# Optimization experiments

Measured on AMD Instinct MI355X. Metric: run time of the kernel, lower is better.

The kernel has to match this reference:

```python
import jax, jax.numpy as jnp
import numpy as np

# Dimensions (AlphaFold-scale IPA / GeometricFrameAttention)
B, N = 1, 768
C_S, C_Z, C_H, H, PQ, PV = 384, 128, 16, 12, 4, 8
INF = 1e9
EPS = 1e-8
SOFTPLUS_INV_1 = 0.541324854612918  # gfa_point_weights_init_


def quat_to_rot(q):
    """Unit-normalize quaternions [..., 4] -> rotation matrices [..., 3, 3]."""
    q = q / jnp.linalg.norm(q, axis=-1, keepdims=True)
    w, x, y, z = q[..., 0], q[..., 1], q[..., 2], q[..., 3]
    R = jnp.stack([
        1 - 2 * (y * y + z * z), 2 * (x * y - w * z), 2 * (x * z + w * y),
        2 * (x * y + w * z), 1 - 2 * (x * x + z * z), 2 * (y * z - w * x),
        2 * (x * z - w * y), 2 * (y * z + w * x), 1 - 2 * (x * x + y * y),
    ], axis=-1)
    return R.reshape(q.shape[:-1] + (3, 3))


def setup_inputs() -> dict:
    key = jax.random.key(0)
    ks = jax.random.split(key, 12)

    def lin(k, out_d, in_d):
        return jax.random.normal(k, (out_d, in_d), jnp.float32) * (1.0 / np.sqrt(in_d))

    out_in = H * C_H + H * PV * 4 + H * C_Z  # o + o_pt(x,y,z) + o_pt_norm + o_pair
    inp = {
        "s": jax.random.normal(ks[0], (B, N, C_S), jnp.float32),
        "z": jax.random.normal(ks[1], (B, N, N, C_Z), jnp.float32),
        "rot": quat_to_rot(jax.random.normal(ks[2], (B, N, 4), jnp.float32)),
        "trans": jax.random.normal(ks[3], (B, N, 3), jnp.float32),
        "mask": jnp.ones((B, N), jnp.float32),
        "Wq": lin(ks[4], H * C_H, C_S),
        "bq": jnp.zeros((H * C_H,), jnp.float32),
        "Wkv": lin(ks[5], H * 2 * C_H, C_S),
        "bkv": jnp.zeros((H * 2 * C_H,), jnp.float32),
        "Wqp": lin(ks[6], H * PQ * 3, C_S),
        "bqp": jnp.zeros((H * PQ * 3,), jnp.float32),
        "Wkvp": lin(ks[7], H * (PQ + PV) * 3, C_S),
        "bkvp": jnp.zeros((H * (PQ + PV) * 3,), jnp.float32),
        "Wb": lin(ks[8], H, C_Z),
        "bb": jnp.zeros((H,), jnp.float32),
        "head_w": jnp.full((H,), SOFTPLUS_INV_1, jnp.float32),
        "Wout": lin(ks[9], C_S, out_in),
        "bout": jnp.zeros((C_S,), jnp.float32),
    }
    return inp


def _forward(s, z, rot, trans, mask, Wq, bq, Wkv, bkv, Wqp, bqp, Wkvp, bkvp,
             Wb, bb, head_w, Wout, bout):
    Bn, Nn, _ = s.shape
    # scalar q/k/v
    q = (s @ Wq.T + bq).reshape(Bn, Nn, H, C_H)
    kv = (s @ Wkv.T + bkv).reshape(Bn, Nn, H, 2 * C_H)
    k, v = kv[..., :C_H], kv[..., C_H:]
    # point q/k/v: local frame -> global frame (x_glob = R x_loc + t)
    q_pts = (s @ Wqp.T + bqp).reshape(Bn, Nn, H * PQ, 3)
    q_pts = (jnp.einsum('bnxy,bnpy->bnpx', rot, q_pts) + trans[:, :, None]).reshape(Bn, Nn, H, PQ, 3)
    kv_pts = (s @ Wkvp.T + bkvp).reshape(Bn, Nn, H * (PQ + PV), 3)
    kv_pts = (jnp.einsum('bnxy,bnpy->bnpx', rot, kv_pts) + trans[:, :, None]).reshape(Bn, Nn, H, PQ + PV, 3)
    k_pts, v_pts = kv_pts[..., :PQ, :], kv_pts[..., PQ:, :]
    # pair bias [B,N,N,H] -> [B,H,N,N]
    bias = z @ Wb.T + bb
    a = jnp.einsum('bihc,bjhc->bhij', q, k) * np.float32(np.sqrt(1.0 / (3 * C_H)))
    a = a + np.float32(np.sqrt(1.0 / 3.0)) * jnp.transpose(bias, (0, 3, 1, 2))
    # point distance term: sum_p |q_p - k_p|^2 = |q|^2 + |k|^2 - 2 q.k (no [B,N,N,H,P,3] tensor)
    q2 = jnp.sum(q_pts ** 2, axis=(-1, -2))  # [B,N,H]
    k2 = jnp.sum(k_pts ** 2, axis=(-1, -2))
    qk = jnp.einsum('bihpc,bjhpc->bhij', q_pts, k_pts)
    d2 = q2.transpose(0, 2, 1)[..., :, None] + k2.transpose(0, 2, 1)[..., None, :] - 2.0 * qk
    hw = jax.nn.softplus(head_w) * np.float32(np.sqrt(2.0 / (27.0 * PQ)))  # sqrt(1/(3*(PQ*9/2)))
    a = a - 0.5 * hw[None, :, None, None] * d2
    # mask bias
    sq_mask = mask[..., :, None] * mask[..., None, :]
    a = a + (INF * (sq_mask - 1.0))[:, None]
    a = jax.nn.softmax(a, axis=-1)  # [B,H,N,N]
    # outputs
    o = jnp.einsum('bhij,bjhc->bihc', a, v).reshape(Bn, Nn, H * C_H)
    o_pt = jnp.einsum('bhij,bjhpc->bihpc', a, v_pts)  # global frame
    o_pt = jnp.einsum('bnyx,bnhpy->bnhpx', rot, o_pt - trans[:, :, None, None])  # back to local
    o_pt_norm = jnp.sqrt(jnp.sum(o_pt ** 2, axis=-1) + EPS).reshape(Bn, Nn, H * PV)
    o_pt_flat = jnp.moveaxis(o_pt, -1, -3).reshape(Bn, Nn, 3 * H * PV)  # coord-major like unbind+cat
    o_pair = jnp.einsum('bhij,bijc->bihc', a, z).reshape(Bn, Nn, H * C_Z)
    cat = jnp.concatenate([o, o_pt_flat, o_pt_norm, o_pair], axis=-1)
    return cat @ Wout.T + bout


def reference(s, z, rot, trans, mask, Wq, bq, Wkv, bkv, Wqp, bqp, Wkvp, bkvp,
              Wb, bb, head_w, Wout, bout):
    return _forward(s, z, rot, trans, mask, Wq, bq, Wkv, bkv, Wqp, bqp,
                    Wkvp, bkvp, Wb, bb, head_w, Wout, bout)
```

## Files before the change

### kernel.cpp

```cpp
#include <hip/hip_runtime.h>
#include <math.h>

#define NN 768
#define CS 384
#define CZ 128
#define CH 16
#define HH 12
#define PQ 4
#define PV 8
#define OUTIN 2112

#define SC_QK 0.14433756729740643f
#define SC_B  0.57735026918962576f
#define SC_HW 0.13608276348795434f
#define MSLACK 12.0f

__device__ __forceinline__ float dpp_add(float x, const int ctrl) {
    int yi;
    switch (ctrl) {
        case 0: yi = __builtin_amdgcn_update_dpp(0, __float_as_int(x), 0xB1,  0xf, 0xf, true); break;
        case 1: yi = __builtin_amdgcn_update_dpp(0, __float_as_int(x), 0x4E,  0xf, 0xf, true); break;
        case 2: yi = __builtin_amdgcn_update_dpp(0, __float_as_int(x), 0x141, 0xf, 0xf, true); break;
        default:yi = __builtin_amdgcn_update_dpp(0, __float_as_int(x), 0x140, 0xf, 0xf, true); break;
    }
    return x + __int_as_float(yi);
}
__device__ __forceinline__ float dpp_max(float x, const int ctrl) {
    int yi;
    switch (ctrl) {
        case 0: yi = __builtin_amdgcn_update_dpp(0, __float_as_int(x), 0xB1,  0xf, 0xf, true); break;
        case 1: yi = __builtin_amdgcn_update_dpp(0, __float_as_int(x), 0x4E,  0xf, 0xf, true); break;
        case 2: yi = __builtin_amdgcn_update_dpp(0, __float_as_int(x), 0x141, 0xf, 0xf, true); break;
        default:yi = __builtin_amdgcn_update_dpp(0, __float_as_int(x), 0x140, 0xf, 0xf, true); break;
    }
    return fmaxf(x, __int_as_float(yi));
}

__global__ __launch_bounds__(256) void kproj(
    const float* __restrict__ s,
    const float* __restrict__ Wq,  const float* __restrict__ bq,
    const float* __restrict__ Wkv, const float* __restrict__ bkv,
    const float* __restrict__ Wqp, const float* __restrict__ bqp,
    const float* __restrict__ Wkvp,const float* __restrict__ bkvp,
    float* __restrict__ q, float* __restrict__ kT, float* __restrict__ vall,
    float* __restrict__ qpr, float* __restrict__ kvpr)
{
    __shared__ float s_lds[8*384];
    int n0 = blockIdx.x * 8;
    int t = threadIdx.x;
    for (int idx = t; idx < 8*384; idx += 256)
        s_lds[idx] = s[(n0 + idx/384)*384 + (idx%384)];
    __syncthreads();

    int o = blockIdx.y * 128 + (t & 127);
    int ng = t >> 7;
    const float* wrow; float bias;
    if (o < 192)      { wrow = Wq   + o*384;       bias = bq[o]; }
    else if (o < 576) { wrow = Wkv  + (o-192)*384; bias = bkv[o-192]; }
    else if (o < 720) { wrow = Wqp  + (o-576)*384; bias = bqp[o-576]; }
    else              { wrow = Wkvp + (o-720)*384; bias = bkvp[o-720]; }

    float acc[4] = {bias, bias, bias, bias};
    const float4* wr4 = reinterpret_cast<const float4*>(wrow);
    for (int c4 = 0; c4 < 96; ++c4) {
        float4 w = wr4[c4];
        #pragma unroll
        for (int nn = 0; nn < 4; ++nn) {
            const float* sr = &s_lds[(ng*4+nn)*384 + c4*4];
            acc[nn] = fmaf(w.x, sr[0], acc[nn]);
            acc[nn] = fmaf(w.y, sr[1], acc[nn]);
            acc[nn] = fmaf(w.z, sr[2], acc[nn]);
            acc[nn] = fmaf(w.w, sr[3], acc[nn]);
        }
    }
    #pragma unroll
    for (int nn = 0; nn < 4; ++nn) {
        int n = n0 + ng*4 + nn;
        float v = acc[nn];
        if (o < 192)      q[n*192 + o] = v;
        else if (o < 576) {
            int oo = o - 192, h = oo >> 5, cc = oo & 31;
            if (cc < 16) kT[(h*NN + n)*16 + cc] = v;
            else         vall[(size_t)n*480 + h*40 + (cc-16)] = v;
        }
        else if (o < 720) qpr[n*144 + (o-576)] = v;
        else              kvpr[n*432 + (o-720)] = v;
    }
}

__global__ __launch_bounds__(192) void krot(
    const float* __restrict__ rot, const float* __restrict__ trans,
    const float* __restrict__ qpr, const float* __restrict__ kvpr,
    float* __restrict__ qp, float* __restrict__ kpT, float* __restrict__ vall)
{
    int n = blockIdx.x;
    __shared__ float R[9], T[3];
    int t = threadIdx.x;
    if (t < 9) R[t] = rot[n*9 + t];
    if (t < 3) T[t] = trans[n*3 + t];
    __syncthreads();

    const float* src = (t < 48) ? (qpr + n*144 + t*3) : (kvpr + n*432 + (t-48)*3);
    float x = src[0], y = src[1], z = src[2];
    float wx = R[0]*x + R[1]*y + R[2]*z + T[0];
    float wy = R[3]*x + R[4]*y + R[5]*z + T[1];
    float wz = R[6]*x + R[7]*y + R[8]*z + T[2];
    if (t < 48) {
        float* d = qp + n*144 + t*3;
        d[0]=wx; d[1]=wy; d[2]=wz;
    } else {
        int pi = t - 48, h = pi/12, pp = pi%12;
        if (pp < 4) {
            float* d = kpT + (h*NN+n)*12 + pp*3;
            d[0]=wx; d[1]=wy; d[2]=wz;
        } else {
            float* d = vall + (size_t)n*480 + h*40 + 16 + (pp-4)*3;
            d[0]=wx; d[1]=wy; d[2]=wz;
        }
    }
}

__global__ __launch_bounds__(256) void kqk(
    const float* __restrict__ kT, const float* __restrict__ kpT,
    const float* __restrict__ q, const float* __restrict__ qp,
    const float* __restrict__ mask, const float* __restrict__ head_w,
    const float* __restrict__ bb, float* __restrict__ lqd,
    float* __restrict__ mpart)
{
    const int j0 = blockIdx.x * 64;
    const int i0 = blockIdx.y * 32;
    __shared__ float ktl[64][17], kpl[64][13];
    __shared__ float ql[32][17],  qpl[32][13];
    __shared__ float mi_l[32], mj_l[64];
    __shared__ float mpl[32][12];
    const int t = threadIdx.x;
    if (t < 32) mi_l[t] = mask[i0 + t];
    if (t < 64) mj_l[t] = mask[j0 + t];

    const int jl = t & 63, wv = t >> 6;

    for (int h = 0; h < 12; ++h) {
        __syncthreads();
        for (int idx = t; idx < 1024; idx += 256)
            ktl[idx >> 4][idx & 15] = kT[(size_t)(h*NN + j0 + (idx >> 4))*16 + (idx & 15)];
        for (int idx = t; idx < 768; idx += 256) {
            int r = idx / 12, e = idx - r*12;
            kpl[r][e] = kpT[(size_t)(h*NN + j0 + r)*12 + e];
        }
        for (int idx = t; idx < 512; idx += 256)
            ql[idx >> 4][idx & 15] = q[(i0 + (idx >> 4))*192 + h*16 + (idx & 15)];
        for (int idx = t; idx < 384; idx += 256) {
            int r = idx / 12, e = idx - r*12;
            qpl[r][e] = qp[(i0 + r)*144 + h*12 + e];
        }
        __syncthreads();

        const float hwh = log1pf(expf(head_w[h])) * SC_HW;
        const float bbh = bb[h] * SC_B;
        const float mj = mj_l[jl];
        #pragma unroll
        for (int k = 0; k < 8; ++k) {
            const int il = wv*8 + k;
            float qk = 0.f;
            #pragma unroll
            for (int c = 0; c < 16; ++c) qk = fmaf(ktl[jl][c], ql[il][c], qk);
            float d2 = 0.f;
            #pragma unroll
            for (int e = 0; e < 12; ++e) { float d = qpl[il][e] - kpl[jl][e]; d2 = fmaf(d, d, d2); }
            float mt = 1e9f * (mi_l[il]*mj - 1.0f);
            float lg = fmaf(qk, SC_QK, fmaf(-0.5f*hwh, d2, bbh)) + mt;
            lqd[((size_t)(i0+il)*NN + j0 + jl)*12 + h] = lg;
            float m = lg;
            m = dpp_max(m, 0);
            m = dpp_max(m, 1);
            m = dpp_max(m, 2);
            m = dpp_max(m, 3);
            m = fmaxf(m, __shfl_xor(m, 16, 64));
            m = fmaxf(m, __shfl_xor(m, 32, 64));
            if (jl == 0) mpl[il][h] = m;
        }
    }
    __syncthreads();
    if (t < 384) {
        int il = t / 12, h = t - il*12;
        mpart[((size_t)h*NN + i0 + il)*12 + blockIdx.x] = mpl[il][h];
    }
}

__global__ __launch_bounds__(256) void kfuse(
    const float* __restrict__ z, const float* __restrict__ Wb,
    const float* __restrict__ lqd, const float* __restrict__ mpart,
    const float* __restrict__ vall,
    float* __restrict__ opart, float* __restrict__ vpart, float* __restrict__ ssum)
{
    __shared__ float  M_lds[12];
    __shared__ __align__(16) float p_lds[12][68];
    __shared__ float2 ofold[4][12][64];
    __shared__ float  sredL[16][6];

    const int i = blockIdx.x, jseg = blockIdx.y;
    const int t = threadIdx.x, w = t >> 6, l = t & 63;
    const int gid = t >> 4, cl = t & 15;
    const int hhalf = gid & 1, h0 = hhalf * 6, jofs = gid >> 1;

    if (t < 12) {
        const float4* mp = (const float4*)(mpart + ((size_t)t*NN + i)*12);
        float4 a = mp[0], b = mp[1], c = mp[2];
        float m = fmaxf(fmaxf(fmaxf(a.x,a.y), fmaxf(a.z,a.w)),
                 fmaxf(fmaxf(fmaxf(b.x,b.y), fmaxf(b.z,b.w)),
                       fmaxf(fmaxf(c.x,c.y), fmaxf(c.z,c.w))));
        M_lds[t] = m + MSLACK;
    }

    float4 wva[6], wvb[6];
    #pragma unroll
    for (int h = 0; h < 6; ++h) {
        const float4* wp = (const float4*)(Wb + (h0+h)*CZ + cl*8);
        wva[h] = wp[0]; wvb[h] = wp[1];
    }

    float2 oa[12];
    #pragma unroll
    for (int h = 0; h < 12; ++h) { oa[h].x = 0.f; oa[h].y = 0.f; }
    float2 vacc; vacc.x = 0.f; vacc.y = 0.f;
    const int vch = 2*t;
    const int vh  = (t < 240) ? (vch / 40) : 0;
    float s_acc = 0.f;

    __syncthreads();
    const float Mh = M_lds[h0 + (cl < 6 ? cl : 5)];
    const int jbase = jseg * 384;

    for (int tile = 0; tile < 6; ++tile) {
        const int jt = jbase + tile*64;

        {
            const float4* zq0 = (const float4*)(z + ((size_t)i*NN + jt + jofs)*CZ) + cl*2;
            float4 za = zq0[0], zb = zq0[1];
            for (int it = 0; it < 8; ++it) {
                float4 zaN = za, zbN = zb;
                if (it + 1 < 8) {
                    const float4* zq = (const float4*)(z + ((size_t)i*NN + jt + (it+1)*8 + jofs)*CZ) + cl*2;
                    zaN = zq[0]; zbN = zq[1];
                }
                const int j = jt + it*8 + jofs;
                float b0, b1, b2, b3, b4, b5;
                #define BDOT(BV, H)                                \
                    BV = za.x*wva[H].x;                            \
                    BV = fmaf(za.y, wva[H].y, BV);                 \
                    BV = fmaf(za.z, wva[H].z, BV);                 \
                    BV = fmaf(za.w, wva[H].w, BV);                 \
                    BV = fmaf(zb.x, wvb[H].x, BV);                 \
                    BV = fmaf(zb.y, wvb[H].y, BV);                 \
                    BV = fmaf(zb.z, wvb[H].z, BV);                 \
                    BV = fmaf(zb.w, wvb[H].w, BV);
                BDOT(b0, 0) BDOT(b1, 1) BDOT(b2, 2) BDOT(b3, 3) BDOT(b4, 4) BDOT(b5, 5)
                #undef BDOT
                #define BRED(BV)                                   \
                    BV = dpp_add(BV, 0);                           \
                    BV = dpp_add(BV, 1);                           \
                    BV = dpp_add(BV, 2);                           \
                    BV = dpp_add(BV, 3);
                BRED(b0) BRED(b1) BRED(b2) BRED(b3) BRED(b4) BRED(b5)
                #undef BRED
                float bsel = b0;
                bsel = (cl == 1) ? b1 : bsel;
                bsel = (cl == 2) ? b2 : bsel;
                bsel = (cl == 3) ? b3 : bsel;
                bsel = (cl == 4) ? b4 : bsel;
                bsel = (cl == 5) ? b5 : bsel;
                if (cl < 6) {
                    float g = fmaf(bsel, SC_B, lqd[((size_t)i*NN + j)*12 + h0 + cl]);
                    float p = __expf(g - Mh);
                    p_lds[h0 + cl][j - jt] = p;
                    s_acc += p;
                }
                za = zaN; zb = zbN;
            }
        }
        __syncthreads();

        {
            const float2* zr2 = (const float2*)(z + (size_t)i*NN*CZ) + l;
            #pragma unroll 4
            for (int jj = 0; jj < 16; ++jj) {
                const int jb = jj*4 + w;
                float2 zv = zr2[(size_t)(jt + jb)*64];
                #pragma unroll
                for (int h = 0; h < 12; ++h) {
                    float pv = p_lds[h][jb];
                    oa[h].x = fmaf(pv, zv.x, oa[h].x);
                    oa[h].y = fmaf(pv, zv.y, oa[h].y);
                }
            }
        }

        if (t < 240) {
            const float2* vr = (const float2*)(vall + (size_t)jt*480 + vch);
            #pragma unroll 4
            for (int q4 = 0; q4 < 16; ++q4) {
                float4 pv = *(const float4*)&p_lds[vh][q4*4];
                float2 v0 = vr[(size_t)(q4*4+0)*240];
                float2 v1 = vr[(size_t)(q4*4+1)*240];
                float2 v2 = vr[(size_t)(q4*4+2)*240];
                float2 v3 = vr[(size_t)(q4*4+3)*240];
                vacc.x = fmaf(pv.x, v0.x, vacc.x); vacc.y = fmaf(pv.x, v0.y, vacc.y);
                vacc.x = fmaf(pv.y, v1.x, vacc.x); vacc.y = fmaf(pv.y, v1.y, vacc.y);
                vacc.x = fmaf(pv.z, v2.x, vacc.x); vacc.y = fmaf(pv.z, v2.y, vacc.y);
                vacc.x = fmaf(pv.w, v3.x, vacc.x); vacc.y = fmaf(pv.w, v3.y, vacc.y);
            }
        }
        __syncthreads();
    }

    #pragma unroll
    for (int h = 0; h < 12; ++h) ofold[w][h][l] = oa[h];
    if (cl < 6) sredL[gid][cl] = s_acc;
    if (t < 240)
        *((float2*)(vpart + ((size_t)(jseg*NN + i))*480) + t) = vacc;
    __syncthreads();

    float2* opw = (float2*)(opart + ((size_t)(jseg*NN + i))*1536);
    #pragma unroll
    for (int k = 0; k < 3; ++k) {
        int slot = k*256 + t;
        int h = slot >> 6, c2 = slot & 63;
        float2 v0 = ofold[0][h][c2], v1 = ofold[1][h][c2];
        float2 v2 = ofold[2][h][c2], v3 = ofold[3][h][c2];
        float2 o;
        o.x = v0.x + v1.x + v2.x + v3.x;
        o.y = v0.y + v1.y + v2.y + v3.y;
        opw[slot] = o;
    }
    if (t < 12) {
        float sv = 0.f;
        #pragma unroll
        for (int k = 0; k < 8; ++k) sv += sredL[k*2 + (t/6)][t % 6];
        ssum[(size_t)(jseg*12 + t)*NN + i] = sv;
    }
}

__global__ __launch_bounds__(256) void kepi(
    const float* __restrict__ opart, const float* __restrict__ vpart,
    const float* __restrict__ ssum, const float* __restrict__ rot,
    const float* __restrict__ trans, float* __restrict__ cat)
{
    __shared__ float sinv[12];
    __shared__ float optl[12][24];
    __shared__ float R[9], T[3];
    const int i = blockIdx.x, t = threadIdx.x;
    if (t < 9) R[t] = rot[i*9 + t];
    if (t < 3) T[t] = trans[i*3 + t];
    if (t >= 16 && t < 28) {
        int h = t - 16;
        sinv[h] = 1.0f / (ssum[(size_t)h*NN + i] + ssum[(size_t)(12+h)*NN + i]);
    }
    __syncthreads();

    float* crow = cat + (size_t)i*OUTIN;
    const float2* op0 = (const float2*)(opart + (size_t)i*1536);
    const float2* op1 = (const float2*)(opart + (size_t)(NN + i)*1536);
    #pragma unroll
    for (int k = 0; k < 3; ++k) {
        int slot = k*256 + t;
        int h = slot >> 6, c2 = slot & 63;
        float2 a = op0[slot], b = op1[slot];
        float sc = sinv[h];
        float2 o; o.x = (a.x + b.x)*sc; o.y = (a.y + b.y)*sc;
        *(float2*)(crow + 576 + h*128 + c2*2) = o;
    }
    if (t < 240) {
        const int ch = 2*t, h = ch/40, e = ch%40;
        float2 v0 = *(const float2*)(vpart + (size_t)i*480 + ch);
        float2 v1 = *(const float2*)(vpart + (size_t)(NN + i)*480 + ch);
        float sc = sinv[h];
        float vx = (v0.x + v1.x)*sc, vy = (v0.y + v1.y)*sc;
        if (e < 16) { crow[h*16 + e] = vx; crow[h*16 + e + 1] = vy; }
        else        { optl[h][e-16] = vx; optl[h][e-15] = vy; }
    }
    __syncthreads();
    if (t < 96) {
        int h = t >> 3, pp = t & 7;
        float wx = optl[h][pp*3+0] - T[0];
        float wy = optl[h][pp*3+1] - T[1];
        float wz = optl[h][pp*3+2] - T[2];
        crow[192 + 0*96 + h*8 + pp] = R[0]*wx + R[3]*wy + R[6]*wz;
        crow[192 + 1*96 + h*8 + pp] = R[1]*wx + R[4]*wy + R[7]*wz;
        crow[192 + 2*96 + h*8 + pp] = R[2]*wx + R[5]*wy + R[8]*wz;
        crow[480 + h*8 + pp] = sqrtf(fmaf(wx,wx,fmaf(wy,wy,wz*wz)) + 1e-8f);
    }
}

__global__ __launch_bounds__(256) void koutp(
    const float* __restrict__ cat, const float* __restrict__ Wout,
    float* __restrict__ ptmp)
{
    __shared__ float ct[32][36];
    __shared__ float wt[64][36];
    const int n0 = blockIdx.x * 32, o0 = blockIdx.y * 64;
    const int k0 = blockIdx.z * 352;
    const int t = threadIdx.x;
    const int tn = (t >> 4) * 2;
    const int to = t & 15;

    float a00=0,a01=0,a02=0,a03=0, a10=0,a11=0,a12=0,a13=0;

    for (int c = 0; c < 11; ++c) {
        __syncthreads();
        #pragma unroll
        for (int u = 0; u < 4; ++u) {
            int idx = u*256 + t, r = idx >> 5, cc = idx & 31;
            ct[r][cc] = cat[(size_t)(n0 + r)*OUTIN + k0 + c*32 + cc];
        }
        #pragma unroll
        for (int u = 0; u < 8; ++u) {
            int idx = u*256 + t, r = idx >> 5, cc = idx & 31;
            wt[r][cc] = Wout[(size_t)(o0 + r)*OUTIN + k0 + c*32 + cc];
        }
        __syncthreads();
        #pragma unroll
        for (int kk = 0; kk < 32; kk += 4) {
            float4 c0 = *(const float4*)&ct[tn][kk];
            float4 c1 = *(const float4*)&ct[tn+1][kk];
            float4 w0 = *(const float4*)&wt[to][kk];
            float4 w1 = *(const float4*)&wt[to+16][kk];
            float4 w2 = *(const float4*)&wt[to+32][kk];
            float4 w3 = *(const float4*)&wt[to+48][kk];
            a00 = fmaf(c0.x,w0.x,a00); a00 = fmaf(c0.y,w0.y,a00); a00 = fmaf(c0.z,w0.z,a00); a00 = fmaf(c0.w,w0.w,a00);
            a01 = fmaf(c0.x,w1.x,a01); a01 = fmaf(c0.y,w1.y,a01); a01 = fmaf(c0.z,w1.z,a01); a01 = fmaf(c0.w,w1.w,a01);
            a02 = fmaf(c0.x,w2.x,a02); a02 = fmaf(c0.y,w2.y,a02); a02 = fmaf(c0.z,w2.z,a02); a02 = fmaf(c0.w,w2.w,a02);
            a03 = fmaf(c0.x,w3.x,a03); a03 = fmaf(c0.y,w3.y,a03); a03 = fmaf(c0.z,w3.z,a03); a03 = fmaf(c0.w,w3.w,a03);
            a10 = fmaf(c1.x,w0.x,a10); a10 = fmaf(c1.y,w0.y,a10); a10 = fmaf(c1.z,w0.z,a10); a10 = fmaf(c1.w,w0.w,a10);
            a11 = fmaf(c1.x,w1.x,a11); a11 = fmaf(c1.y,w1.y,a11); a11 = fmaf(c1.z,w1.z,a11); a11 = fmaf(c1.w,w1.w,a11);
            a12 = fmaf(c1.x,w2.x,a12); a12 = fmaf(c1.y,w2.y,a12); a12 = fmaf(c1.z,w2.z,a12); a12 = fmaf(c1.w,w2.w,a12);
            a13 = fmaf(c1.x,w3.x,a13); a13 = fmaf(c1.y,w3.y,a13); a13 = fmaf(c1.z,w3.z,a13); a13 = fmaf(c1.w,w3.w,a13);
        }
    }
    float* pb = ptmp + (size_t)blockIdx.z * (NN*384);
    pb[(size_t)(n0+tn+0)*384 + o0+to+ 0] = a00;
    pb[(size_t)(n0+tn+0)*384 + o0+to+16] = a01;
    pb[(size_t)(n0+tn+0)*384 + o0+to+32] = a02;
    pb[(size_t)(n0+tn+0)*384 + o0+to+48] = a03;
    pb[(size_t)(n0+tn+1)*384 + o0+to+ 0] = a10;
    pb[(size_t)(n0+tn+1)*384 + o0+to+16] = a11;
    pb[(size_t)(n0+tn+1)*384 + o0+to+32] = a12;
    pb[(size_t)(n0+tn+1)*384 + o0+to+48] = a13;
}

__global__ __launch_bounds__(256) void kred(
    const float* __restrict__ ptmp, const float* __restrict__ bout,
    float* __restrict__ out)
{
    int idx = blockIdx.x * 256 + threadIdx.x;
    int o = idx % 384;
    float v = bout[o];
    #pragma unroll
    for (int s = 0; s < 6; ++s) v += ptmp[(size_t)s*(NN*384) + idx];
    out[idx] = v;
}

extern "C" void kernel_launch(void* const* d_in, const int* in_sizes, int n_in,
                              void* d_out, int out_size, void* d_ws, size_t ws_size,
                              hipStream_t stream) {
    const float* s      = (const float*)d_in[0];
    const float* z      = (const float*)d_in[1];
    const float* rot    = (const float*)d_in[2];
    const float* trans  = (const float*)d_in[3];
    const float* mask   = (const float*)d_in[4];
    const float* Wq     = (const float*)d_in[5];
    const float* bq     = (const float*)d_in[6];
    const float* Wkv    = (const float*)d_in[7];
    const float* bkv    = (const float*)d_in[8];
    const float* Wqp    = (const float*)d_in[9];
    const float* bqp    = (const float*)d_in[10];
    const float* Wkvp   = (const float*)d_in[11];
    const float* bkvp   = (const float*)d_in[12];
    const float* Wb     = (const float*)d_in[13];
    const float* bb     = (const float*)d_in[14];
    const float* head_w = (const float*)d_in[15];
    const float* Wout   = (const float*)d_in[16];
    const float* bout   = (const float*)d_in[17];
    float* out = (float*)d_out;
    float* ws  = (float*)d_ws;

    float* q     = ws;
    float* kT    = ws + 147456;
    float* kpT   = ws + 294912;
    float* vall  = ws + 405504;
    float* qp    = ws + 774144;
    float* qpr   = ws + 884736;
    float* kvpr  = ws + 995328;
    float* mpart = ws + 1327104;
    float* ssum  = ws + 1437696;
    float* cat   = ws + 1456128;
    float* lqd   = ws + 3078144;
    float* opart = ws + 10156032;
    float* vpart = ws + 12515328;
    float* ptmp  = ws + 13252608;

    kproj<<<dim3(96, 9), 256, 0, stream>>>(s, Wq, bq, Wkv, bkv, Wqp, bqp, Wkvp, bkvp,
                                           q, kT, vall, qpr, kvpr);
    krot<<<dim3(768), 192, 0, stream>>>(rot, trans, qpr, kvpr, qp, kpT, vall);
    kqk<<<dim3(12, 24), 256, 0, stream>>>(kT, kpT, q, qp, mask, head_w, bb, lqd, mpart);
    kfuse<<<dim3(768, 2), 256, 0, stream>>>(z, Wb, lqd, mpart, vall, opart, vpart, ssum);
    kepi<<<dim3(768), 256, 0, stream>>>(opart, vpart, ssum, rot, trans, cat);
    koutp<<<dim3(24, 6, 6), 256, 0, stream>>>(cat, Wout, ptmp);
    kred<<<dim3(1152), 256, 0, stream>>>(ptmp, bout, out);
}
```

Before: 402.0 us.

## Split kfuse over four j-segments and read transposed probabilities as float4

The fused pair-bias/softmax/aggregation kernel now splits the key dimension into four segments of 192 instead of two of 384, which doubles the grid to 3072 blocks. The epilogue now sums four partial outputs and four partial row sums. Probabilities are also written to a transposed LDS buffer, so the z-aggregation loop reads them with three float4 loads instead of twelve scalar loads. The workspace layout is reordered to fit the larger partial buffers, with ptmp aliased onto lqd. The trade-offs are more partial-sum traffic in kepi, extra LDS stores, and more LDS per block.

After: 411.2 us. 2.3% more time.

```diff
diff --git a/kernel.cpp b/kernel.cpp
--- a/kernel.cpp
+++ b/kernel.cpp
@@ -195,6 +195,7 @@
 {
     __shared__ float  M_lds[12];
     __shared__ __align__(16) float p_lds[12][68];
+    __shared__ __align__(16) float p_T[64][16];
     __shared__ float2 ofold[4][12][64];
     __shared__ float  sredL[16][6];
 
@@ -229,9 +230,9 @@
 
     __syncthreads();
     const float Mh = M_lds[h0 + (cl < 6 ? cl : 5)];
-    const int jbase = jseg * 384;
-
-    for (int tile = 0; tile < 6; ++tile) {
+    const int jbase = jseg * 192;
+
+    for (int tile = 0; tile < 3; ++tile) {
         const int jt = jbase + tile*64;
 
         {
@@ -273,6 +274,7 @@
                     float g = fmaf(bsel, SC_B, lqd[((size_t)i*NN + j)*12 + h0 + cl]);
                     float p = __expf(g - Mh);
                     p_lds[h0 + cl][j - jt] = p;
+                    p_T[j - jt][h0 + cl] = p;
                     s_acc += p;
                 }
                 za = zaN; zb = zbN;
@@ -286,12 +288,21 @@
             for (int jj = 0; jj < 16; ++jj) {
                 const int jb = jj*4 + w;
                 float2 zv = zr2[(size_t)(jt + jb)*64];
-                #pragma unroll
-                for (int h = 0; h < 12; ++h) {
-                    float pv = p_lds[h][jb];
-                    oa[h].x = fmaf(pv, zv.x, oa[h].x);
-                    oa[h].y = fmaf(pv, zv.y, oa[h].y);
-                }
+                float4 pA = *(const float4*)&p_T[jb][0];
+                float4 pB = *(const float4*)&p_T[jb][4];
+                float4 pC = *(const float4*)&p_T[jb][8];
+                oa[0].x  = fmaf(pA.x, zv.x, oa[0].x);  oa[0].y  = fmaf(pA.x, zv.y, oa[0].y);
+                oa[1].x  = fmaf(pA.y, zv.x, oa[1].x);  oa[1].y  = fmaf(pA.y, zv.y, oa[1].y);
+                oa[2].x  = fmaf(pA.z, zv.x, oa[2].x);  oa[2].y  = fmaf(pA.z, zv.y, oa[2].y);
+                oa[3].x  = fmaf(pA.w, zv.x, oa[3].x);  oa[3].y  = fmaf(pA.w, zv.y, oa[3].y);
+                oa[4].x  = fmaf(pB.x, zv.x, oa[4].x);  oa[4].y  = fmaf(pB.x, zv.y, oa[4].y);
+                oa[5].x  = fmaf(pB.y, zv.x, oa[5].x);  oa[5].y  = fmaf(pB.y, zv.y, oa[5].y);
+                oa[6].x  = fmaf(pB.z, zv.x, oa[6].x);  oa[6].y  = fmaf(pB.z, zv.y, oa[6].y);
+                oa[7].x  = fmaf(pB.w, zv.x, oa[7].x);  oa[7].y  = fmaf(pB.w, zv.y, oa[7].y);
+                oa[8].x  = fmaf(pC.x, zv.x, oa[8].x);  oa[8].y  = fmaf(pC.x, zv.y, oa[8].y);
+                oa[9].x  = fmaf(pC.y, zv.x, oa[9].x);  oa[9].y  = fmaf(pC.y, zv.y, oa[9].y);
+                oa[10].x = fmaf(pC.z, zv.x, oa[10].x); oa[10].y = fmaf(pC.z, zv.y, oa[10].y);
+                oa[11].x = fmaf(pC.w, zv.x, oa[11].x); oa[11].y = fmaf(pC.w, zv.y, oa[11].y);
             }
         }
 
@@ -353,28 +364,36 @@
     if (t < 3) T[t] = trans[i*3 + t];
     if (t >= 16 && t < 28) {
         int h = t - 16;
-        sinv[h] = 1.0f / (ssum[(size_t)h*NN + i] + ssum[(size_t)(12+h)*NN + i]);
+        sinv[h] = 1.0f / (ssum[(size_t)h*NN + i] + ssum[(size_t)(12+h)*NN + i]
+                        + ssum[(size_t)(24+h)*NN + i] + ssum[(size_t)(36+h)*NN + i]);
     }
     __syncthreads();
 
     float* crow = cat + (size_t)i*OUTIN;
     const float2* op0 = (const float2*)(opart + (size_t)i*1536);
     const float2* op1 = (const float2*)(opart + (size_t)(NN + i)*1536);
+    const float2* op2 = (const float2*)(opart + (size_t)(2*NN + i)*1536);
+    const float2* op3 = (const float2*)(opart + (size_t)(3*NN + i)*1536);
     #pragma unroll
     for (int k = 0; k < 3; ++k) {
         int slot = k*256 + t;
         int h = slot >> 6, c2 = slot & 63;
-        float2 a = op0[slot], b = op1[slot];
+        float2 a = op0[slot], b = op1[slot], c = op2[slot], d = op3[slot];
         float sc = sinv[h];
-        float2 o; o.x = (a.x + b.x)*sc; o.y = (a.y + b.y)*sc;
+        float2 o;
+        o.x = (a.x + b.x + c.x + d.x)*sc;
+        o.y = (a.y + b.y + c.y + d.y)*sc;
         *(float2*)(crow + 576 + h*128 + c2*2) = o;
     }
     if (t < 240) {
         const int ch = 2*t, h = ch/40, e = ch%40;
         float2 v0 = *(const float2*)(vpart + (size_t)i*480 + ch);
         float2 v1 = *(const float2*)(vpart + (size_t)(NN + i)*480 + ch);
+        float2 v2 = *(const float2*)(vpart + (size_t)(2*NN + i)*480 + ch);
+        float2 v3 = *(const float2*)(vpart + (size_t)(3*NN + i)*480 + ch);
         float sc = sinv[h];
-        float vx = (v0.x + v1.x)*sc, vy = (v0.y + v1.y)*sc;
+        float vx = (v0.x + v1.x + v2.x + v3.x)*sc;
+        float vy = (v0.y + v1.y + v2.y + v3.y)*sc;
         if (e < 16) { crow[h*16 + e] = vx; crow[h*16 + e + 1] = vy; }
         else        { optl[h][e-16] = vx; optl[h][e-15] = vy; }
     }
@@ -483,26 +502,26 @@
     float* out = (float*)d_out;
     float* ws  = (float*)d_ws;
 
-    float* q     = ws;
-    float* kT    = ws + 147456;
-    float* kpT   = ws + 294912;
-    float* vall  = ws + 405504;
-    float* qp    = ws + 774144;
-    float* qpr   = ws + 884736;
-    float* kvpr  = ws + 995328;
-    float* mpart = ws + 1327104;
-    float* ssum  = ws + 1437696;
-    float* cat   = ws + 1456128;
-    float* lqd   = ws + 3078144;
-    float* opart = ws + 10156032;
-    float* vpart = ws + 12515328;
-    float* ptmp  = ws + 13252608;
+    float* vall  = ws;
+    float* mpart = ws + 368640;
+    float* ssum  = ws + 479232;
+    float* cat   = ws + 516096;
+    float* lqd   = ws + 2138112;
+    float* opart = ws + 9216000;
+    float* vpart = ws + 13934592;
+    float* q     = ws + 15409152;
+    float* kT    = ws + 15556608;
+    float* kpT   = ws + 15704064;
+    float* qp    = ws + 15814656;
+    float* qpr   = ws + 15925248;
+    float* kvpr  = ws + 16035840;
+    float* ptmp  = lqd;
 
     kproj<<<dim3(96, 9), 256, 0, stream>>>(s, Wq, bq, Wkv, bkv, Wqp, bqp, Wkvp, bkvp,
                                            q, kT, vall, qpr, kvpr);
     krot<<<dim3(768), 192, 0, stream>>>(rot, trans, qpr, kvpr, qp, kpT, vall);
     kqk<<<dim3(12, 24), 256, 0, stream>>>(kT, kpT, q, qp, mask, head_w, bb, lqd, mpart);
-    kfuse<<<dim3(768, 2), 256, 0, stream>>>(z, Wb, lqd, mpart, vall, opart, vpart, ssum);
+    kfuse<<<dim3(768, 4), 256, 0, stream>>>(z, Wb, lqd, mpart, vall, opart, vpart, ssum);
     kepi<<<dim3(768), 256, 0, stream>>>(opart, vpart, ssum, rot, trans, cat);
     koutp<<<dim3(24, 6, 6), 256, 0, stream>>>(cat, Wout, ptmp);
     kred<<<dim3(1152), 256, 0, stream>>>(ptmp, bout, out);
```
